# Performance work log

Measured on AMD Instinct MI355X. Metric: run time of the kernel, lower is better.

Reference implementation:

```python
import jax, jax.numpy as jnp
import numpy as np

B, S, D = 4, 2048, 1024
E, K, H = 8, 2, 4096


def setup_inputs() -> dict:
    key = jax.random.key(0)
    ks = jax.random.split(key, 8)
    sd = 1.0 / np.sqrt(D)
    sh = 1.0 / np.sqrt(H)
    x = jax.random.normal(ks[0], (B, S, D), dtype=jnp.float32)
    gate_w = jax.random.normal(ks[1], (D, E), dtype=jnp.float32) * sd
    gate_b = jnp.zeros((E,), dtype=jnp.float32)
    w1 = jax.random.normal(ks[2], (E, D, H), dtype=jnp.float32) * sd
    b1 = jnp.zeros((E, H), dtype=jnp.float32)
    w2 = jax.random.normal(ks[3], (E, H, D), dtype=jnp.float32) * sh
    b2 = jnp.zeros((E, D), dtype=jnp.float32)
    return {"x": x, "gate_w": gate_w, "gate_b": gate_b,
            "w1": w1, "b1": b1, "w2": w2, "b2": b2}


def reference(x, gate_w, gate_b, w1, b1, w2, b2):
    # gate logits [B,S,E]
    logits = jnp.einsum('bsd,de->bse', x, gate_w) + gate_b
    # top-k over experts, softmax over the k selected (dim=2), in float32
    weights, selected = jax.lax.top_k(logits, K)            # [B,S,K]
    weights = jax.nn.softmax(weights.astype(jnp.float32), axis=-1).astype(x.dtype)
    out = jnp.zeros_like(x)
    for i in range(E):
        # per-token combine weight for expert i (0 if not routed here)
        w_i = jnp.sum(jnp.where(selected == i, weights, 0.0), axis=-1)  # [B,S]
        h = jax.nn.gelu(jnp.einsum('bsd,dh->bsh', x, w1[i]) + b1[i])    # [B,S,H]
        y = jnp.einsum('bsh,hd->bsd', h, w2[i]) + b2[i]                  # [B,S,D]
        out = out + w_i[..., None] * y
    return out
```

## Files before the change

kernel.cpp:

```cpp
#include <hip/hip_runtime.h>
#include <hip/hip_bf16.h>
#include <stdint.h>

#define T_TOK 8192
#define D_DIM 1024
#define E_NUM 8
#define H_DIM 4096
#define NPAD 144
#define PPX (NPAD / 8)

typedef short bf16x8 __attribute__((ext_vector_type(8)));
typedef float f32x4 __attribute__((ext_vector_type(4)));

#define AS1 __attribute__((address_space(1)))
#define AS3 __attribute__((address_space(3)))

__device__ __forceinline__ unsigned short f2b(float f) {
  union { float f; uint32_t u; } v; v.f = f;
  uint32_t r = (v.u + 0x7fffu + ((v.u >> 16) & 1u)) >> 16;
  return (unsigned short)r;
}

__device__ __forceinline__ float gelu_tanh(float x) {
  float u = 0.7978845608028654f * (x + 0.044715f * x * x * x);
  u = fminf(fmaxf(u, -15.f), 15.f);
  float e = __expf(2.f * u);
  float t = (e - 1.f) / (e + 1.f);
  return 0.5f * x * (1.f + t);
}

__device__ __forceinline__ void gload_lds16(const void* g, void* l) {
  __builtin_amdgcn_global_load_lds((const AS1 uint32_t*)g, (AS3 uint32_t*)l, 16, 0, 0);
}

__global__ __launch_bounds__(256) void moe_gate_conv(const float* __restrict__ x,
                                                     const float* __restrict__ gw,
                                                     const float* __restrict__ gb,
                                                     unsigned short* __restrict__ xb,
                                                     int2* __restrict__ sel,
                                                     float2* __restrict__ wts,
                                                     int* __restrict__ meta) {
  int lane = threadIdx.x & 63;
  int t = blockIdx.x * 4 + (threadIdx.x >> 6);
  const float* xr = x + (size_t)t * D_DIM;
  unsigned short* xo = xb + (size_t)t * D_DIM;
  float acc[8];
#pragma unroll
  for (int e = 0; e < 8; e++) acc[e] = 0.f;
#pragma unroll
  for (int i = 0; i < 4; i++) {
    int d0 = lane * 4 + i * 256;
    float4 xv = *(const float4*)(xr + d0);
    ushort4 o;
    o.x = f2b(xv.x); o.y = f2b(xv.y); o.z = f2b(xv.z); o.w = f2b(xv.w);
    *(ushort4*)(xo + d0) = o;
    const float* gp = gw + (size_t)d0 * 8;
    float xs[4] = {xv.x, xv.y, xv.z, xv.w};
#pragma unroll
    for (int j = 0; j < 4; j++) {
#pragma unroll
      for (int e = 0; e < 8; e++) acc[e] += xs[j] * gp[j * 8 + e];
    }
  }
#pragma unroll
  for (int off = 32; off > 0; off >>= 1) {
#pragma unroll
    for (int e = 0; e < 8; e++) acc[e] += __shfl_xor(acc[e], off);
  }
  if (lane == 0) {
    float lg[8];
#pragma unroll
    for (int e = 0; e < 8; e++) lg[e] = acc[e] + gb[e];
    int e0 = 0; float b0 = lg[0];
#pragma unroll
    for (int e = 1; e < 8; e++) if (lg[e] > b0) { b0 = lg[e]; e0 = e; }
    int e1 = -1; float b1v = -1e30f;
#pragma unroll
    for (int e = 0; e < 8; e++) if (e != e0 && lg[e] > b1v) { b1v = lg[e]; e1 = e; }
    float d = __expf(b1v - b0);
    float w0 = 1.f / (1.f + d), w1 = d / (1.f + d);
    sel[t] = make_int2(e0, e1);
    wts[t] = make_float2(w0, w1);
    atomicAdd(&meta[e0], 1);
    atomicAdd(&meta[e1], 1);
  }
}

__global__ __launch_bounds__(256) void moe_transpose(const float* __restrict__ in,
                                                     unsigned short* __restrict__ out,
                                                     int R, int C) {
  int e = blockIdx.z;
  int c0 = blockIdx.x * 64, r0 = blockIdx.y * 64;
  __shared__ float tile[64][65];
  const float* ine = in + (size_t)e * R * C;
  unsigned short* oute = out + (size_t)e * R * C;
  int tr = threadIdx.x >> 2;
  int tc4 = (threadIdx.x & 3) * 16;
#pragma unroll
  for (int p = 0; p < 4; p++) {
    int c = tc4 + p * 4;
    float4 v = *(const float4*)(ine + (size_t)(r0 + tr) * C + c0 + c);
    tile[tr][c] = v.x; tile[tr][c + 1] = v.y; tile[tr][c + 2] = v.z; tile[tr][c + 3] = v.w;
  }
  __syncthreads();
#pragma unroll
  for (int p = 0; p < 4; p++) {
    int rr = tc4 + p * 4;
    ushort4 o;
    o.x = f2b(tile[rr + 0][tr]);
    o.y = f2b(tile[rr + 1][tr]);
    o.z = f2b(tile[rr + 2][tr]);
    o.w = f2b(tile[rr + 3][tr]);
    *(ushort4*)(oute + (size_t)(c0 + tr) * R + r0 + rr) = o;
  }
}

__global__ void moe_scan(int* meta, int2* wl) {
  if (threadIdx.x == 0 && blockIdx.x == 0) {
    int o = 0;
    for (int e = 0; e < 8; e++) { meta[8 + e] = o; meta[20 + e] = o; o += meta[e]; }
    meta[16] = o;
    int w = 0;
    for (int e = 0; e < 8; e++)
      for (int m0 = 0; m0 < meta[e]; m0 += 128) wl[w++] = make_int2(e, m0);
    meta[17] = w;
  }
}

__global__ __launch_bounds__(256) void moe_scatter(const int2* __restrict__ sel,
                                                   const float2* __restrict__ wts,
                                                   int* __restrict__ meta,
                                                   int* __restrict__ token_id,
                                                   float* __restrict__ weightv) {
  int t = blockIdx.x * 256 + threadIdx.x;
  if (t >= T_TOK) return;
  int2 s = sel[t];
  float2 w = wts[t];
  int p0 = atomicAdd(&meta[20 + s.x], 1); token_id[p0] = t; weightv[p0] = w.x;
  int p1 = atomicAdd(&meta[20 + s.y], 1); token_id[p1] = t; weightv[p1] = w.y;
}

__global__ __launch_bounds__(256) void moe_outinit(const int2* __restrict__ sel,
                                                   const float2* __restrict__ wts,
                                                   const float* __restrict__ b2,
                                                   float* __restrict__ out) {
  int t = blockIdx.x;
  int d = threadIdx.x * 4;
  int2 s = sel[t];
  float2 w = wts[t];
  float4 a = *(const float4*)(b2 + (size_t)s.x * D_DIM + d);
  float4 b = *(const float4*)(b2 + (size_t)s.y * D_DIM + d);
  float4 o;
  o.x = w.x * a.x + w.y * b.x;
  o.y = w.x * a.y + w.y * b.y;
  o.z = w.x * a.z + w.y * b.z;
  o.w = w.x * a.w + w.y * b.w;
  *(float4*)(out + (size_t)t * D_DIM + d) = o;
}

__global__ __launch_bounds__(256) void moe_gemm1(const unsigned short* __restrict__ xb,
                                                 const unsigned short* __restrict__ w1t,
                                                 const float* __restrict__ b1,
                                                 const int* __restrict__ meta,
                                                 const int2* __restrict__ wl,
                                                 const int* __restrict__ token_id,
                                                 unsigned short* __restrict__ hbuf) {
  int b = blockIdx.x;
  int c = b & 7, u = b >> 3;
  int n = u & 31, ps = u >> 5;
  int wi = c * PPX + ps;
  if (wi >= meta[17]) return;
  int e = wl[wi].x, m0 = wl[wi].y;
  int seg = meta[8 + e], ne = meta[9 + e] - seg;
  int n0 = n * 128;
  const unsigned short* wB = w1t + (size_t)e * H_DIM * D_DIM;

  __shared__ unsigned short As[2][4096];
  __shared__ unsigned short Bs[2][4096];

  int tid = threadIdx.x, lane = tid & 63, wv = tid >> 6;
  const unsigned short* aptr[2];
  const unsigned short* bptr[2];
#pragma unroll
  for (int q = 0; q < 2; q++) {
    int chunk = (wv + 4 * q) * 64 + lane;
    int row = chunk >> 2;
    int ko = (chunk & 3) * 8;
    int gi = m0 + row; if (gi >= ne) gi = m0;
    int tok = token_id[seg + gi];
    aptr[q] = xb + (size_t)tok * D_DIM + ko;
    bptr[q] = wB + (size_t)(n0 + row) * D_DIM + ko;
  }
  auto stage = [&](int buf, int kt) {
#pragma unroll
    for (int q = 0; q < 2; q++) {
      gload_lds16(aptr[q] + kt * 32, &As[buf][(wv + 4 * q) * 512]);
      gload_lds16(bptr[q] + kt * 32, &Bs[buf][(wv + 4 * q) * 512]);
    }
  };

  f32x4 acc[4][4] = {};
  int wr = wv >> 1, wc = wv & 1;
  int abase = (wr * 64 + (lane & 15)) * 32 + (lane >> 4) * 8;
  int bbase = (wc * 64 + (lane & 15)) * 32 + (lane >> 4) * 8;

  stage(0, 0);
  __syncthreads();
  const int nk = D_DIM / 32;
  for (int kt = 0; kt < nk; ++kt) {
    int cur = kt & 1;
    if (kt + 1 < nk) stage(cur ^ 1, kt + 1);
    bf16x8 af[4], bfr[4];
#pragma unroll
    for (int m = 0; m < 4; m++) af[m] = *(const bf16x8*)&As[cur][abase + m * 512];
#pragma unroll
    for (int nn = 0; nn < 4; nn++) bfr[nn] = *(const bf16x8*)&Bs[cur][bbase + nn * 512];
#pragma unroll
    for (int m = 0; m < 4; m++)
#pragma unroll
      for (int nn = 0; nn < 4; nn++)
        acc[m][nn] = __builtin_amdgcn_mfma_f32_16x16x32_bf16(af[m], bfr[nn], acc[m][nn], 0, 0, 0);
    __syncthreads();
  }

  int rbase = wr * 64 + (lane >> 4) * 4;
  int cbase = n0 + wc * 64 + (lane & 15);
  const float* b1e = b1 + (size_t)e * H_DIM + cbase;
  float bv[4];
#pragma unroll
  for (int nn = 0; nn < 4; nn++) bv[nn] = b1e[nn * 16];
#pragma unroll
  for (int m = 0; m < 4; m++) {
#pragma unroll
    for (int j = 0; j < 4; j++) {
      int gi = m0 + rbase + m * 16 + j;
      if (gi < ne) {
        unsigned short* hrow = hbuf + (size_t)(seg + gi) * H_DIM + cbase;
#pragma unroll
        for (int nn = 0; nn < 4; nn++) {
          float v = acc[m][nn][j] + bv[nn];
          hrow[nn * 16] = f2b(gelu_tanh(v));
        }
      }
    }
  }
}

__global__ __launch_bounds__(256) void moe_gemm2(const unsigned short* __restrict__ hbuf,
                                                 const unsigned short* __restrict__ w2t,
                                                 const int* __restrict__ meta,
                                                 const int2* __restrict__ wl,
                                                 const int* __restrict__ token_id,
                                                 const float* __restrict__ weightv,
                                                 float* __restrict__ out) {
  int b = blockIdx.x;
  int c = b & 7, u = b >> 3;
  int n = u & 7, ps = u >> 3;
  int wi = c * PPX + ps;
  if (wi >= meta[17]) return;
  int e = wl[wi].x, m0 = wl[wi].y;
  int seg = meta[8 + e], ne = meta[9 + e] - seg;
  int n0 = n * 128;
  const unsigned short* wB = w2t + (size_t)e * D_DIM * H_DIM;

  __shared__ unsigned short As[2][4096];
  __shared__ unsigned short Bs[2][4096];

  int tid = threadIdx.x, lane = tid & 63, wv = tid >> 6;
  const unsigned short* aptr[2];
  const unsigned short* bptr[2];
#pragma unroll
  for (int q = 0; q < 2; q++) {
    int chunk = (wv + 4 * q) * 64 + lane;
    int row = chunk >> 2;
    int ko = (chunk & 3) * 8;
    int gi = m0 + row; if (gi >= ne) gi = m0;
    aptr[q] = hbuf + (size_t)(seg + gi) * H_DIM + ko;
    bptr[q] = wB + (size_t)(n0 + row) * H_DIM + ko;
  }
  auto stage = [&](int buf, int kt) {
#pragma unroll
    for (int q = 0; q < 2; q++) {
      gload_lds16(aptr[q] + kt * 32, &As[buf][(wv + 4 * q) * 512]);
      gload_lds16(bptr[q] + kt * 32, &Bs[buf][(wv + 4 * q) * 512]);
    }
  };

  f32x4 acc[4][4] = {};
  int wr = wv >> 1, wc = wv & 1;
  int abase = (wr * 64 + (lane & 15)) * 32 + (lane >> 4) * 8;
  int bbase = (wc * 64 + (lane & 15)) * 32 + (lane >> 4) * 8;

  stage(0, 0);
  __syncthreads();
  const int nk = H_DIM / 32;
  for (int kt = 0; kt < nk; ++kt) {
    int cur = kt & 1;
    if (kt + 1 < nk) stage(cur ^ 1, kt + 1);
    bf16x8 af[4], bfr[4];
#pragma unroll
    for (int m = 0; m < 4; m++) af[m] = *(const bf16x8*)&As[cur][abase + m * 512];
#pragma unroll
    for (int nn = 0; nn < 4; nn++) bfr[nn] = *(const bf16x8*)&Bs[cur][bbase + nn * 512];
#pragma unroll
    for (int m = 0; m < 4; m++)
#pragma unroll
      for (int nn = 0; nn < 4; nn++)
        acc[m][nn] = __builtin_amdgcn_mfma_f32_16x16x32_bf16(af[m], bfr[nn], acc[m][nn], 0, 0, 0);
    __syncthreads();
  }

  int rbase = wr * 64 + (lane >> 4) * 4;
  int cbase = n0 + wc * 64 + (lane & 15);
#pragma unroll
  for (int m = 0; m < 4; m++) {
#pragma unroll
    for (int j = 0; j < 4; j++) {
      int gi = m0 + rbase + m * 16 + j;
      if (gi < ne) {
        int p = seg + gi;
        int tok = token_id[p];
        float wt = weightv[p];
        float* orow = out + (size_t)tok * D_DIM + cbase;
#pragma unroll
        for (int nn = 0; nn < 4; nn++)
          atomicAdd(&orow[nn * 16], wt * acc[m][nn][j]);
      }
    }
  }
}

extern "C" void kernel_launch(void* const* d_in, const int* in_sizes, int n_in,
                              void* d_out, int out_size, void* d_ws, size_t ws_size,
                              hipStream_t stream) {
  const float* x      = (const float*)d_in[0];
  const float* gate_w = (const float*)d_in[1];
  const float* gate_b = (const float*)d_in[2];
  const float* w1     = (const float*)d_in[3];
  const float* b1     = (const float*)d_in[4];
  const float* w2     = (const float*)d_in[5];
  const float* b2     = (const float*)d_in[6];
  float* out = (float*)d_out;

  uint8_t* ws = (uint8_t*)d_ws;
  unsigned short* hbuf = (unsigned short*)(ws);
  unsigned short* xb   = (unsigned short*)(ws + 134217728ull);
  unsigned short* w1t  = (unsigned short*)(ws + 150994944ull);
  unsigned short* w2t  = (unsigned short*)(ws + 218103808ull);
  int*    token_id = (int*)  (ws + 285212672ull);
  float*  weightv  = (float*)(ws + 285278208ull);
  float2* wts      = (float2*)(ws + 285343744ull);
  int2*   sel      = (int2*) (ws + 285409280ull);
  int*    meta     = (int*)  (ws + 285474816ull);
  int2*   wl       = (int2*) (ws + 285475328ull);

  hipMemsetAsync(meta, 0, 512, stream);

  moe_gate_conv<<<dim3(T_TOK / 4), 256, 0, stream>>>(x, gate_w, gate_b, xb, sel, wts, meta);
  moe_transpose<<<dim3(H_DIM / 64, D_DIM / 64, E_NUM), 256, 0, stream>>>(w1, w1t, D_DIM, H_DIM);
  moe_transpose<<<dim3(D_DIM / 64, H_DIM / 64, E_NUM), 256, 0, stream>>>(w2, w2t, H_DIM, D_DIM);
  moe_scan<<<1, 64, 0, stream>>>(meta, wl);
  moe_scatter<<<dim3(T_TOK / 256), 256, 0, stream>>>(sel, wts, meta, token_id, weightv);
  moe_outinit<<<dim3(T_TOK), 256, 0, stream>>>(sel, wts, b2, out);

  moe_gemm1<<<dim3(NPAD * 32), 256, 0, stream>>>(xb, w1t, b1, meta, wl, token_id, hbuf);
  moe_gemm2<<<dim3(NPAD * 8), 256, 0, stream>>>(hbuf, w2t, meta, wl, token_id, weightv, out);
}
```

Measured before the change: 889.3 us.

## Merge weight transposes, fold bias into gemm2, deepen gemm2 K-tile to 64

Merges the two weight transpose launches into one kernel and reworks its access pattern to coalesce reads and write 16-byte bf16 vectors. Drops the output-init kernel: output is memset to zero and the second-layer bias is added, scaled by the routing weight, inside gemm2's atomic epilogue. gemm2 now stages 64-wide K slices per barrier (double LDS footprint) to halve the number of syncs. The chunk index in both GEMM load setups is rewritten in a form that computes the same value.

```diff
diff --git a/kernel.cpp b/kernel.cpp
--- a/kernel.cpp
+++ b/kernel.cpp
@@ -11,6 +11,7 @@
 
 typedef short bf16x8 __attribute__((ext_vector_type(8)));
 typedef float f32x4 __attribute__((ext_vector_type(4)));
+typedef unsigned short usv8 __attribute__((ext_vector_type(8)));
 
 #define AS1 __attribute__((address_space(1)))
 #define AS3 __attribute__((address_space(3)))
@@ -86,32 +87,36 @@
   }
 }
 
-__global__ __launch_bounds__(256) void moe_transpose(const float* __restrict__ in,
-                                                     unsigned short* __restrict__ out,
-                                                     int R, int C) {
-  int e = blockIdx.z;
-  int c0 = blockIdx.x * 64, r0 = blockIdx.y * 64;
+__global__ __launch_bounds__(256) void moe_transpose2(const float* __restrict__ w1,
+                                                      const float* __restrict__ w2,
+                                                      unsigned short* __restrict__ w1t,
+                                                      unsigned short* __restrict__ w2t) {
+  int z = blockIdx.y;
+  int e = z & 7;
+  const float* in; unsigned short* out; int R, C, cy, ry;
+  if (z < 8) { in = w1 + (size_t)e * D_DIM * H_DIM; out = w1t + (size_t)e * D_DIM * H_DIM;
+               R = D_DIM; C = H_DIM; cy = blockIdx.x & 63; ry = blockIdx.x >> 6; }
+  else       { in = w2 + (size_t)e * H_DIM * D_DIM; out = w2t + (size_t)e * H_DIM * D_DIM;
+               R = H_DIM; C = D_DIM; cy = blockIdx.x & 15; ry = blockIdx.x >> 4; }
+  int r0 = ry * 64, c0 = cy * 64;
   __shared__ float tile[64][65];
-  const float* ine = in + (size_t)e * R * C;
-  unsigned short* oute = out + (size_t)e * R * C;
-  int tr = threadIdx.x >> 2;
-  int tc4 = (threadIdx.x & 3) * 16;
-#pragma unroll
-  for (int p = 0; p < 4; p++) {
-    int c = tc4 + p * 4;
-    float4 v = *(const float4*)(ine + (size_t)(r0 + tr) * C + c0 + c);
-    tile[tr][c] = v.x; tile[tr][c + 1] = v.y; tile[tr][c + 2] = v.z; tile[tr][c + 3] = v.w;
+  int t = threadIdx.x;
+  int ir = t >> 4, ic = (t & 15) * 4;
+#pragma unroll
+  for (int p = 0; p < 4; ++p) {
+    float4 v = *(const float4*)(in + (size_t)(r0 + ir + p * 16) * C + c0 + ic);
+    tile[ir + p * 16][ic] = v.x;     tile[ir + p * 16][ic + 1] = v.y;
+    tile[ir + p * 16][ic + 2] = v.z; tile[ir + p * 16][ic + 3] = v.w;
   }
   __syncthreads();
-#pragma unroll
-  for (int p = 0; p < 4; p++) {
-    int rr = tc4 + p * 4;
-    ushort4 o;
-    o.x = f2b(tile[rr + 0][tr]);
-    o.y = f2b(tile[rr + 1][tr]);
-    o.z = f2b(tile[rr + 2][tr]);
-    o.w = f2b(tile[rr + 3][tr]);
-    *(ushort4*)(oute + (size_t)(c0 + tr) * R + r0 + rr) = o;
+  int orow = t >> 3, oc = (t & 7) * 8;
+#pragma unroll
+  for (int q = 0; q < 2; ++q) {
+    int r = orow + q * 32;
+    usv8 o;
+#pragma unroll
+    for (int j = 0; j < 8; ++j) o[j] = f2b(tile[oc + j][r]);
+    *(usv8*)(out + (size_t)(c0 + r) * R + r0 + oc) = o;
   }
 }
 
@@ -138,24 +143,6 @@
   float2 w = wts[t];
   int p0 = atomicAdd(&meta[20 + s.x], 1); token_id[p0] = t; weightv[p0] = w.x;
   int p1 = atomicAdd(&meta[20 + s.y], 1); token_id[p1] = t; weightv[p1] = w.y;
-}
-
-__global__ __launch_bounds__(256) void moe_outinit(const int2* __restrict__ sel,
-                                                   const float2* __restrict__ wts,
-                                                   const float* __restrict__ b2,
-                                                   float* __restrict__ out) {
-  int t = blockIdx.x;
-  int d = threadIdx.x * 4;
-  int2 s = sel[t];
-  float2 w = wts[t];
-  float4 a = *(const float4*)(b2 + (size_t)s.x * D_DIM + d);
-  float4 b = *(const float4*)(b2 + (size_t)s.y * D_DIM + d);
-  float4 o;
-  o.x = w.x * a.x + w.y * b.x;
-  o.y = w.x * a.y + w.y * b.y;
-  o.z = w.x * a.z + w.y * b.z;
-  o.w = w.x * a.w + w.y * b.w;
-  *(float4*)(out + (size_t)t * D_DIM + d) = o;
 }
 
 __global__ __launch_bounds__(256) void moe_gemm1(const unsigned short* __restrict__ xb,
@@ -183,7 +170,7 @@
   const unsigned short* bptr[2];
 #pragma unroll
   for (int q = 0; q < 2; q++) {
-    int chunk = (wv + 4 * q) * 64 + lane;
+    int chunk = tid + q * 256;
     int row = chunk >> 2;
     int ko = (chunk & 3) * 8;
     int gi = m0 + row; if (gi >= ne) gi = m0;
@@ -248,6 +235,7 @@
 
 __global__ __launch_bounds__(256) void moe_gemm2(const unsigned short* __restrict__ hbuf,
                                                  const unsigned short* __restrict__ w2t,
+                                                 const float* __restrict__ b2,
                                                  const int* __restrict__ meta,
                                                  const int2* __restrict__ wl,
                                                  const int* __restrict__ token_id,
@@ -263,15 +251,15 @@
   int n0 = n * 128;
   const unsigned short* wB = w2t + (size_t)e * D_DIM * H_DIM;
 
-  __shared__ unsigned short As[2][4096];
-  __shared__ unsigned short Bs[2][4096];
+  __shared__ unsigned short As[2][8192];
+  __shared__ unsigned short Bs[2][8192];
 
   int tid = threadIdx.x, lane = tid & 63, wv = tid >> 6;
   const unsigned short* aptr[2];
   const unsigned short* bptr[2];
 #pragma unroll
   for (int q = 0; q < 2; q++) {
-    int chunk = (wv + 4 * q) * 64 + lane;
+    int chunk = tid + q * 256;
     int row = chunk >> 2;
     int ko = (chunk & 3) * 8;
     int gi = m0 + row; if (gi >= ne) gi = m0;
@@ -280,10 +268,12 @@
   }
   auto stage = [&](int buf, int kt) {
 #pragma unroll
-    for (int q = 0; q < 2; q++) {
-      gload_lds16(aptr[q] + kt * 32, &As[buf][(wv + 4 * q) * 512]);
-      gload_lds16(bptr[q] + kt * 32, &Bs[buf][(wv + 4 * q) * 512]);
-    }
+    for (int ks = 0; ks < 2; ks++)
+#pragma unroll
+      for (int q = 0; q < 2; q++) {
+        gload_lds16(aptr[q] + kt * 64 + ks * 32, &As[buf][ks * 4096 + (wv + 4 * q) * 512]);
+        gload_lds16(bptr[q] + kt * 64 + ks * 32, &Bs[buf][ks * 4096 + (wv + 4 * q) * 512]);
+      }
   };
 
   f32x4 acc[4][4] = {};
@@ -293,25 +283,32 @@
 
   stage(0, 0);
   __syncthreads();
-  const int nk = H_DIM / 32;
+  const int nk = H_DIM / 64;
   for (int kt = 0; kt < nk; ++kt) {
     int cur = kt & 1;
     if (kt + 1 < nk) stage(cur ^ 1, kt + 1);
-    bf16x8 af[4], bfr[4];
-#pragma unroll
-    for (int m = 0; m < 4; m++) af[m] = *(const bf16x8*)&As[cur][abase + m * 512];
-#pragma unroll
-    for (int nn = 0; nn < 4; nn++) bfr[nn] = *(const bf16x8*)&Bs[cur][bbase + nn * 512];
-#pragma unroll
-    for (int m = 0; m < 4; m++)
-#pragma unroll
-      for (int nn = 0; nn < 4; nn++)
-        acc[m][nn] = __builtin_amdgcn_mfma_f32_16x16x32_bf16(af[m], bfr[nn], acc[m][nn], 0, 0, 0);
+#pragma unroll
+    for (int ks = 0; ks < 2; ks++) {
+      bf16x8 af[4], bfr[4];
+#pragma unroll
+      for (int m = 0; m < 4; m++) af[m] = *(const bf16x8*)&As[cur][ks * 4096 + abase + m * 512];
+#pragma unroll
+      for (int nn = 0; nn < 4; nn++) bfr[nn] = *(const bf16x8*)&Bs[cur][ks * 4096 + bbase + nn * 512];
+#pragma unroll
+      for (int m = 0; m < 4; m++)
+#pragma unroll
+        for (int nn = 0; nn < 4; nn++)
+          acc[m][nn] = __builtin_amdgcn_mfma_f32_16x16x32_bf16(af[m], bfr[nn], acc[m][nn], 0, 0, 0);
+    }
     __syncthreads();
   }
 
   int rbase = wr * 64 + (lane >> 4) * 4;
   int cbase = n0 + wc * 64 + (lane & 15);
+  const float* b2e = b2 + (size_t)e * D_DIM + cbase;
+  float bv[4];
+#pragma unroll
+  for (int nn = 0; nn < 4; nn++) bv[nn] = b2e[nn * 16];
 #pragma unroll
   for (int m = 0; m < 4; m++) {
 #pragma unroll
@@ -324,7 +321,7 @@
         float* orow = out + (size_t)tok * D_DIM + cbase;
 #pragma unroll
         for (int nn = 0; nn < 4; nn++)
-          atomicAdd(&orow[nn * 16], wt * acc[m][nn][j]);
+          atomicAdd(&orow[nn * 16], wt * (acc[m][nn][j] + bv[nn]));
       }
     }
   }
@@ -355,14 +352,13 @@
   int2*   wl       = (int2*) (ws + 285475328ull);
 
   hipMemsetAsync(meta, 0, 512, stream);
+  hipMemsetAsync(out, 0, (size_t)T_TOK * D_DIM * sizeof(float), stream);
 
   moe_gate_conv<<<dim3(T_TOK / 4), 256, 0, stream>>>(x, gate_w, gate_b, xb, sel, wts, meta);
-  moe_transpose<<<dim3(H_DIM / 64, D_DIM / 64, E_NUM), 256, 0, stream>>>(w1, w1t, D_DIM, H_DIM);
-  moe_transpose<<<dim3(D_DIM / 64, H_DIM / 64, E_NUM), 256, 0, stream>>>(w2, w2t, H_DIM, D_DIM);
+  moe_transpose2<<<dim3(1024, 16), 256, 0, stream>>>(w1, w2, w1t, w2t);
   moe_scan<<<1, 64, 0, stream>>>(meta, wl);
   moe_scatter<<<dim3(T_TOK / 256), 256, 0, stream>>>(sel, wts, meta, token_id, weightv);
-  moe_outinit<<<dim3(T_TOK), 256, 0, stream>>>(sel, wts, b2, out);
 
   moe_gemm1<<<dim3(NPAD * 32), 256, 0, stream>>>(xb, w1t, b1, meta, wl, token_id, hbuf);
-  moe_gemm2<<<dim3(NPAD * 8), 256, 0, stream>>>(hbuf, w2t, meta, wl, token_id, weightv, out);
-}
+  moe_gemm2<<<dim3(NPAD * 8), 256, 0, stream>>>(hbuf, w2t, b2, meta, wl, token_id, weightv, out);
+}
```

After: 976.5 us. 9.8% more time.
